# Optimization experiments

Hardware: AMD Instinct MI355X
Metric: run time of the kernel (lower is better)

## Reference

```python
import jax, jax.numpy as jnp
import numpy as np

N_MEM = 50000
MATCH_THR2 = 0.01   # squared-distance match threshold (0.1 m)
EMA = 0.5           # EMA factor for matched-descriptor update
EPS = 1e-8


def _bilinear_depth(depth, uv):
    # depth: [H, W]; uv: [M, 2] pixel coords (u = x/col, v = y/row)
    H, W = depth.shape
    u = jnp.clip(uv[:, 0], 0.0, W - 1.001)
    v = jnp.clip(uv[:, 1], 0.0, H - 1.001)
    u0 = jnp.floor(u); v0 = jnp.floor(v)
    du = u - u0; dv = v - v0
    u0i = u0.astype(jnp.int32); v0i = v0.astype(jnp.int32)
    d00 = depth[v0i, u0i]
    d01 = depth[v0i, u0i + 1]
    d10 = depth[v0i + 1, u0i]
    d11 = depth[v0i + 1, u0i + 1]
    return d00 * (1 - du) * (1 - dv) + d01 * du * (1 - dv) + d10 * (1 - du) * dv + d11 * du * dv


def pix2world(points, depth_map, pose, K):
    # points [B,M,2], depth_map [B,1,H,W], pose [B,3,4] cam->world, K [B,3,3]
    d = jax.vmap(_bilinear_depth)(depth_map[:, 0], points)            # [B,M]
    pix = jnp.concatenate([points, jnp.ones_like(points[..., :1])], -1)  # [B,M,3]
    Kinv = jnp.linalg.inv(K)
    cam = jnp.einsum('bij,bmj->bmi', Kinv, pix) * d[..., None]        # [B,M,3]
    world = jnp.einsum('bij,bmj->bmi', pose[:, :, :3], cam) + pose[:, :, 3][:, None, :]
    valid = (d > 0) & jnp.isfinite(world).all(-1)                      # [B,M]
    return world, valid


def memory_write(pts, desc, valid, mem_pts, mem_desc, next_ptr):
    # pts [P,3], desc [P,D]; mem_pts [N,3], mem_desc [N,D]
    d2 = (jnp.sum(pts * pts, -1, keepdims=True)
          - 2.0 * pts @ mem_pts.T
          + jnp.sum(mem_pts * mem_pts, -1)[None, :])                  # [P,N]
    idx = jnp.argmin(d2, axis=1)                                       # [P]
    dmin = jnp.take_along_axis(d2, idx[:, None], axis=1)[:, 0]
    match = (dmin < MATCH_THR2) & valid
    n_match = match.sum()
    # returned descriptors come from the (non-differentiable) memory buffer;
    # unmatched entries return their own descriptor (cos=1 -> zero loss/grad)
    matched_desc = jax.lax.stop_gradient(jnp.where(match[:, None], mem_desc[idx], desc))
    # --- state update (buffers: no gradient) ---
    dsg = jax.lax.stop_gradient(desc)
    psg = jax.lax.stop_gradient(pts)
    unm = (~match) & valid
    slots = (next_ptr + jnp.cumsum(unm.astype(jnp.int32)) - 1) % N_MEM
    widx = jnp.where(unm, slots, idx)                                  # [P]
    old_pts = mem_pts[widx]; old_desc = mem_desc[widx]
    upd = old_desc * EMA + dsg * (1.0 - EMA)
    upd = upd / (jnp.linalg.norm(upd, axis=-1, keepdims=True) + EPS)
    new_desc_vals = jnp.where(match[:, None], upd, jnp.where(unm[:, None], dsg, old_desc))
    new_pts_vals = jnp.where(unm[:, None], psg, old_pts)
    new_mem_desc = mem_desc.at[widx].set(new_desc_vals)
    new_mem_pts = mem_pts.at[widx].set(new_pts_vals)
    return matched_desc, n_match, new_mem_pts, new_mem_desc


def setup_inputs() -> dict:
    key = jax.random.key(0)
    ks = jax.random.split(key, 8)
    B, M, D, H, W = 8, 512, 256, 480, 640
    points = jax.random.uniform(ks[0], (B, M, 2), jnp.float32) * jnp.array([W - 2.0, H - 2.0])
    depth_map = 0.5 + 4.5 * jax.random.uniform(ks[1], (B, 1, H, W), jnp.float32)
    # proper rotations via QR + small translations
    A = np.asarray(jax.random.normal(ks[2], (B, 3, 3)))
    Rs = np.stack([np.linalg.qr(A[b])[0] for b in range(B)]).astype(np.float32)
    t = np.asarray(jax.random.normal(ks[3], (B, 3, 1))) * 2.0
    pose = jnp.asarray(np.concatenate([Rs, t.astype(np.float32)], axis=2))  # [B,3,4]
    Kmat = jnp.broadcast_to(jnp.array([[320.0, 0.0, 320.0], [0.0, 320.0, 240.0], [0.0, 0.0, 1.0]], jnp.float32), (B, 3, 3))
    descriptors = jax.random.normal(ks[4], (B, M, D), jnp.float32)
    mem_pts = (jax.random.uniform(ks[5], (N_MEM, 3), jnp.float32) - 0.5) * 16.0
    mem_desc = jax.random.normal(ks[6], (N_MEM, D), jnp.float32)
    mem_desc = mem_desc / (jnp.linalg.norm(mem_desc, axis=-1, keepdims=True) + EPS)
    return {"points": points, "depth_map": depth_map, "pose": pose, "K": Kmat,
            "descriptors": descriptors, "mem_pts": mem_pts, "mem_desc": mem_desc,
            "next_ptr": 20000}


def reference(points, depth_map, pose, K, descriptors, mem_pts, mem_desc, next_ptr):
    world, valid = pix2world(points, depth_map, pose, K)               # [B,M,3], [B,M]
    P = world.shape[0] * world.shape[1]
    pts = world.reshape(P, 3)
    desc = descriptors.reshape(P, -1)
    vmask = valid.reshape(P)
    pts = jnp.where(vmask[:, None], pts, 1e6)   # invalid points never match
    matched_desc, n_match, new_mem_pts, new_mem_desc = memory_write(
        pts, desc, vmask, mem_pts, mem_desc, next_ptr)
    a = desc / jnp.maximum(jnp.linalg.norm(desc, axis=-1, keepdims=True), EPS)
    b = matched_desc / jnp.maximum(jnp.linalg.norm(matched_desc, axis=-1, keepdims=True), EPS)
    cos = jnp.sum(a * b, -1)                                           # [P]
    nv = jnp.maximum(vmask.sum(), 1)
    loss = 1.0 - jnp.sum(cos * vmask) / nv
    return loss, n_match, new_mem_pts, new_mem_desc
```

## Files before the change

### kernel.cpp

```cpp
#include <hip/hip_runtime.h>
#include <math.h>

#define N_MEM   50000
#define P_TOT   4096
#define DDIM    256
#define HDIM    480
#define WDIM    640
#define SWEEPB  196
#define COPYB   2048
#define THR2    0.01f
#define EPSF    1e-8f

#define GDIM    24
#define NCELL   13824
#define GORG    -8.25f
#define GINV    (1.0f/0.6875f)
#define GRS     0.15f
#define CPT     14

typedef unsigned long long ull;

__device__ __forceinline__ unsigned fsort(float x) {
    unsigned b = __float_as_uint(x);
    return (b & 0x80000000u) ? ~b : (b | 0x80000000u);
}

__device__ __forceinline__ int cell1d(float x) {
    int c = (int)((x - GORG) * GINV);
    return min(max(c, 0), GDIM - 1);
}

__global__ __launch_bounds__(1024) void k_build(const float* __restrict__ points,
                                                const float* __restrict__ depth,
                                                const float* __restrict__ pose,
                                                const float* __restrict__ Kmat,
                                                float4* __restrict__ pts_out,
                                                int* __restrict__ flags_out,
                                                ull* __restrict__ minkey,
                                                int* __restrict__ qstart,
                                                int* __restrict__ qidx,
                                                ull* __restrict__ minkey_inv,
                                                float* __restrict__ cos_acc)
{
    __shared__ int cnt[NCELL];
    __shared__ int bsum[1024];
    int t = threadIdx.x;
    for (int c = t; c < NCELL; c += 1024) cnt[c] = 0;
    if (t == 0) { *minkey_inv = 0xFFFFFFFFFFFFFFFFULL; *cos_acc = 0.f; }
    for (int k = t; k < P_TOT; k += 1024) minkey[k] = 0xFFFFFFFFFFFFFFFFULL;
    __syncthreads();

    int cells[4];
    #pragma unroll
    for (int i = 0; i < 4; ++i) {
        int p = i * 1024 + t;
        int b = p >> 9;
        const float* K = Kmat + b * 9;
        float a00=K[0],a01=K[1],a02=K[2],a10=K[3],a11=K[4],a12=K[5],a20=K[6],a21=K[7],a22=K[8];
        float det = a00*(a11*a22-a12*a21) - a01*(a10*a22-a12*a20) + a02*(a10*a21-a11*a20);
        float id = 1.0f/det;
        float i00=(a11*a22-a12*a21)*id, i01=(a02*a21-a01*a22)*id, i02=(a01*a12-a02*a11)*id;
        float i10=(a12*a20-a10*a22)*id, i11=(a00*a22-a02*a20)*id, i12=(a02*a10-a00*a12)*id;
        float i20=(a10*a21-a11*a20)*id, i21=(a01*a20-a00*a21)*id, i22=(a00*a11-a01*a10)*id;

        float u = points[p*2+0], v = points[p*2+1];
        float uc = fminf(fmaxf(u, 0.f), (float)WDIM - 1.001f);
        float vc = fminf(fmaxf(v, 0.f), (float)HDIM - 1.001f);
        float u0 = floorf(uc), v0 = floorf(vc);
        float du = uc - u0, dv = vc - v0;
        int u0i = (int)u0, v0i = (int)v0;
        const float* dm = depth + (size_t)b * HDIM * WDIM;
        float d00 = dm[v0i*WDIM + u0i];
        float d01 = dm[v0i*WDIM + u0i + 1];
        float d10 = dm[(v0i+1)*WDIM + u0i];
        float d11 = dm[(v0i+1)*WDIM + u0i + 1];
        float d = d00*(1.f-du)*(1.f-dv) + d01*du*(1.f-dv) + d10*(1.f-du)*dv + d11*du*dv;

        float cx = (i00*u + i01*v + i02) * d;
        float cy = (i10*u + i11*v + i12) * d;
        float cz = (i20*u + i21*v + i22) * d;
        const float* T = pose + b * 12;
        float wx = T[0]*cx + T[1]*cy + T[2]*cz  + T[3];
        float wy = T[4]*cx + T[5]*cy + T[6]*cz  + T[7];
        float wz = T[8]*cx + T[9]*cy + T[10]*cz + T[11];
        int val = (d > 0.f) && isfinite(wx) && isfinite(wy) && isfinite(wz);
        float px = val ? wx : 1e6f;
        float py = val ? wy : 1e6f;
        float pz = val ? wz : 1e6f;
        float pp = px*px + py*py + pz*pz;
        pts_out[p] = make_float4(px, py, pz, pp);
        flags_out[p] = val;
        int c = -1;
        if (val) {
            c = (cell1d(pz) * GDIM + cell1d(py)) * GDIM + cell1d(px);
            atomicAdd(&cnt[c], 1);
        }
        cells[i] = c;
    }
    __syncthreads();

    int base = t * CPT;
    int loc[CPT];
    int sum = 0;
    #pragma unroll
    for (int i = 0; i < CPT; ++i) {
        int idx = base + i;
        int cv = (idx < NCELL) ? cnt[idx] : 0;
        loc[i] = sum; sum += cv;
    }
    bsum[t] = sum;
    __syncthreads();
    for (int off = 1; off < 1024; off <<= 1) {
        int a = bsum[t];
        int bb = (t >= off) ? bsum[t - off] : 0;
        __syncthreads();
        bsum[t] = a + bb;
        __syncthreads();
    }
    int ex = bsum[t] - sum;
    #pragma unroll
    for (int i = 0; i < CPT; ++i) {
        int idx = base + i;
        if (idx < NCELL) { int s0 = ex + loc[i]; qstart[idx] = s0; cnt[idx] = s0; }
    }
    if (t == 1023) qstart[NCELL] = bsum[1023];
    __syncthreads();

    #pragma unroll
    for (int i = 0; i < 4; ++i) {
        if (cells[i] >= 0) {
            int p = i * 1024 + t;
            int pos = atomicAdd(&cnt[cells[i]], 1);
            qidx[pos] = p;
        }
    }
}

__global__ __launch_bounds__(256) void k_main(const float* __restrict__ mem_pts,
                                              const float* __restrict__ mem_desc,
                                              const float4* __restrict__ pts,
                                              const int* __restrict__ qstart,
                                              const int* __restrict__ qidx,
                                              ull* __restrict__ minkey,
                                              ull* __restrict__ minkey_inv,
                                              float* __restrict__ out_pts,
                                              float* __restrict__ out_desc)
{
    __shared__ ull sred[4];
    int bid = blockIdx.x;
    int t = threadIdx.x;
    if (bid < SWEEPB) {
        int j = bid * 256 + t;
        ull ikey = 0xFFFFFFFFFFFFFFFFULL;
        if (j < N_MEM) {
            float mx = mem_pts[j*3+0], my = mem_pts[j*3+1], mz = mem_pts[j*3+2];
            float mm = mx*mx + my*my + mz*mz;
            float px = 1e6f;
            float pp  = px*px + px*px + px*px;
            float dot = px*mx + px*my + px*mz;
            float dinv = pp - 2.f*dot + mm;
            ikey = ((ull)fsort(dinv) << 32) | (unsigned)j;
            int cx0 = cell1d(mx - GRS), cx1 = cell1d(mx + GRS);
            int cy0 = cell1d(my - GRS), cy1 = cell1d(my + GRS);
            int cz0 = cell1d(mz - GRS), cz1 = cell1d(mz + GRS);
            for (int zz = cz0; zz <= cz1; ++zz)
                for (int yy = cy0; yy <= cy1; ++yy) {
                    int rowc = (zz * GDIM + yy) * GDIM;
                    for (int xx = cx0; xx <= cx1; ++xx) {
                        int cell = rowc + xx;
                        int s0 = qstart[cell], s1 = qstart[cell + 1];
                        for (int k = s0; k < s1; ++k) {
                            int p = qidx[k];
                            float4 P = pts[p];
                            float dotq = P.x*mx + P.y*my + P.z*mz;
                            float dd2 = P.w - 2.f*dotq + mm;
                            atomicMin(&minkey[p], ((ull)fsort(dd2) << 32) | (unsigned)j);
                        }
                    }
                }
        }
        for (int off = 32; off; off >>= 1) {
            ull o = __shfl_xor(ikey, off);
            ikey = o < ikey ? o : ikey;
        }
        if ((t & 63) == 0) sred[t >> 6] = ikey;
        __syncthreads();
        if (t == 0) {
            ull a = sred[0] < sred[1] ? sred[0] : sred[1];
            ull b = sred[2] < sred[3] ? sred[2] : sred[3];
            ull m = a < b ? a : b;
            atomicMin(minkey_inv, m);
        }
    } else {
        const long tid = (long)(bid - SWEEPB) * 256 + t;
        const long stride = (long)COPYB * 256;
        const float2* ds = (const float2*)mem_desc;
        float2* dd = (float2*)out_desc;
        const long ND2 = (long)N_MEM * DDIM / 2;
        long k = tid * 4;
        const long stride4 = stride * 4;
        for (; k + 3 < ND2; k += stride4) {
            float2 a0 = ds[k+0], a1 = ds[k+1], a2 = ds[k+2], a3 = ds[k+3];
            dd[k+0] = a0; dd[k+1] = a1; dd[k+2] = a2; dd[k+3] = a3;
        }
        for (; k < ND2; ++k) dd[k] = ds[k];
        const float2* ps = (const float2*)mem_pts;
        float2* pd = (float2*)out_pts;
        for (long i = tid; i < (long)N_MEM * 3 / 2; i += stride) pd[i] = ps[i];
    }
}

__global__ __launch_bounds__(1024) void k_scan(const ull* __restrict__ minkey,
                                               int* __restrict__ flags,
                                               const int* __restrict__ next_ptr,
                                               const ull* __restrict__ minkey_inv,
                                               int* __restrict__ widx,
                                               int* __restrict__ winner,
                                               float* __restrict__ dout,
                                               float* __restrict__ scan_out)
{
    __shared__ int su[1024];
    __shared__ int smc[1024];
    int t = threadIdx.x;
    int base = t * 4;
    const ull thr_key = ((ull)fsort(THR2)) << 32;
    ull inv = *minkey_inv;
    int um[4], iv[4], wvv[4];
    int usum = 0, msum = 0;
    #pragma unroll
    for (int k = 0; k < 4; k++) {
        int v = flags[base + k] & 1;
        ull key = v ? minkey[base + k] : inv;
        int m = (key < thr_key) && v;
        int u = (!m) && v;
        iv[k] = (int)(key & 0xffffffffULL);
        um[k] = u; usum += u; msum += m;
        flags[base + k] = v | (m << 1) | (u << 2);
    }
    su[t] = usum; smc[t] = msum;
    __syncthreads();
    for (int off = 1; off < 1024; off <<= 1) {
        int a = su[t], b = (t >= off) ? su[t - off] : 0;
        int c = smc[t], d = (t >= off) ? smc[t - off] : 0;
        __syncthreads();
        su[t] = a + b; smc[t] = c + d;
        __syncthreads();
    }
    int excl = su[t] - usum;
    int np_ = *next_ptr;
    int run = excl;
    #pragma unroll
    for (int k = 0; k < 4; k++) {
        int wv;
        if (um[k]) { run += 1; wv = (np_ + run - 1) % N_MEM; }
        else       { wv = iv[k]; }
        widx[base + k] = wv;
        wvv[k] = wv;
        winner[wv] = -1;
    }
    __syncthreads();
    #pragma unroll
    for (int k = 0; k < 4; k++)
        atomicMax(&winner[wvv[k]], base + k);
    if (t == 1023) {
        dout[1]     = (float)smc[1023];
        scan_out[0] = (float)(smc[1023] + su[1023]);
        scan_out[1] = (float)su[1023];
    }
}

__global__ __launch_bounds__(256) void k_scatloss(const int* __restrict__ widx,
                                                  const int* __restrict__ flags,
                                                  const int* __restrict__ winner,
                                                  const float* __restrict__ desc,
                                                  const float4* __restrict__ pts,
                                                  const float* __restrict__ mem_pts,
                                                  const float* __restrict__ mem_desc,
                                                  float* __restrict__ out_pts,
                                                  float* __restrict__ out_desc,
                                                  float* __restrict__ cos_acc)
{
    __shared__ float red[16];
    int p = blockIdx.x;
    int t = threadIdx.x;
    int f = flags[p];
    int m = (f >> 1) & 1, u = (f >> 2) & 1;
    int wi = widx[p];
    int win = (winner[wi] == p);
    if (!m && !win) return;
    float dsg = desc[p * DDIM + t];
    float old = mem_desc[(long)wi * DDIM + t];
    float val;
    if (m) {
        float up = old * 0.5f + dsg * 0.5f;
        float sdd = dsg * dsg, smm2 = old * old, sdm = dsg * old, suu = up * up;
        for (int off = 32; off; off >>= 1) {
            sdd  += __shfl_xor(sdd,  off);
            smm2 += __shfl_xor(smm2, off);
            sdm  += __shfl_xor(sdm,  off);
            suu  += __shfl_xor(suu,  off);
        }
        int w = t >> 6;
        if ((t & 63) == 0) { red[w] = sdd; red[4+w] = smm2; red[8+w] = sdm; red[12+w] = suu; }
        __syncthreads();
        float dd  = red[0] + red[1] + red[2] + red[3];
        float mm2 = red[4] + red[5] + red[6] + red[7];
        float dm  = red[8] + red[9] + red[10] + red[11];
        float uu  = red[12] + red[13] + red[14] + red[15];
        float cosv = dm / (fmaxf(sqrtf(dd), EPSF) * fmaxf(sqrtf(mm2), EPSF));
        val = up / (sqrtf(uu) + EPSF);
        if (t == 0) atomicAdd(cos_acc, cosv);
    } else {
        val = u ? dsg : old;
    }
    if (win) {
        out_desc[(long)wi * DDIM + t] = val;
        if (t == 0) {
            float px, py, pz;
            if (u) { float4 P = pts[p]; px = P.x; py = P.y; pz = P.z; }
            else   { px = mem_pts[wi*3]; py = mem_pts[wi*3+1]; pz = mem_pts[wi*3+2]; }
            out_pts[wi*3+0] = px; out_pts[wi*3+1] = py; out_pts[wi*3+2] = pz;
        }
    }
}

__global__ void k_final(const float* __restrict__ cos_acc,
                        const float* __restrict__ scan_out,
                        float* __restrict__ dout)
{
    if (threadIdx.x == 0) {
        float nv = fmaxf(scan_out[0], 1.f);
        dout[0] = 1.f - (*cos_acc + scan_out[1]) / nv;
    }
}

extern "C" void kernel_launch(void* const* d_in, const int* in_sizes, int n_in,
                              void* d_out, int out_size, void* d_ws, size_t ws_size,
                              hipStream_t stream)
{
    const float* points   = (const float*)d_in[0];
    const float* depth    = (const float*)d_in[1];
    const float* pose     = (const float*)d_in[2];
    const float* Kmat     = (const float*)d_in[3];
    const float* desc     = (const float*)d_in[4];
    const float* mem_pts  = (const float*)d_in[5];
    const float* mem_desc = (const float*)d_in[6];
    const int*   next_ptr = (const int*)d_in[7];

    float* out      = (float*)d_out;
    float* out_pts  = out + 2;
    float* out_desc = out + 2 + (long)N_MEM * 3;

    char* ws = (char*)d_ws;
    float4* pts_ws    = (float4*)(ws);
    int* flags_ws     = (int*)(ws + 65536);
    int* widx_ws      = (int*)(ws + 81920);
    int* winner_ws    = (int*)(ws + 98304);
    ull* minkey_ws    = (ull*)(ws + 298304);
    int* qstart_ws    = (int*)(ws + 331072);
    int* qidx_ws      = (int*)(ws + 386372);
    ull* minkey_inv   = (ull*)(ws + 402760);
    float* scan_out   = (float*)(ws + 402768);
    float* cos_acc    = (float*)(ws + 402776);

    k_build   <<<1, 1024, 0, stream>>>(points, depth, pose, Kmat,
                                       pts_ws, flags_ws, minkey_ws,
                                       qstart_ws, qidx_ws, minkey_inv, cos_acc);
    k_main    <<<SWEEPB + COPYB, 256, 0, stream>>>(mem_pts, mem_desc, pts_ws,
                                                   qstart_ws, qidx_ws, minkey_ws, minkey_inv,
                                                   out_pts, out_desc);
    k_scan    <<<1, 1024, 0, stream>>>(minkey_ws, flags_ws, next_ptr, minkey_inv,
                                       widx_ws, winner_ws, out, scan_out);
    k_scatloss<<<P_TOT, 256, 0, stream>>>(widx_ws, flags_ws, winner_ws, desc, pts_ws,
                                          mem_pts, mem_desc, out_pts, out_desc, cos_acc);
    k_final   <<<1, 64, 0, stream>>>(cos_acc, scan_out, out);
}
```

Before: 203.3 us.

## Bin memory points into grid and query per point-cell instead of per memory point

```diff
diff --git a/kernel.cpp b/kernel.cpp
--- a/kernel.cpp
+++ b/kernel.cpp
@@ -6,7 +6,7 @@
 #define DDIM    256
 #define HDIM    480
 #define WDIM    640
-#define SWEEPB  196
+#define SWEEPB  128
 #define COPYB   2048
 #define THR2    0.01f
 #define EPSF    1e-8f
@@ -34,70 +34,91 @@
                                                 const float* __restrict__ depth,
                                                 const float* __restrict__ pose,
                                                 const float* __restrict__ Kmat,
+                                                const float* __restrict__ mem_pts,
                                                 float4* __restrict__ pts_out,
                                                 int* __restrict__ flags_out,
                                                 ull* __restrict__ minkey,
-                                                int* __restrict__ qstart,
-                                                int* __restrict__ qidx,
-                                                ull* __restrict__ minkey_inv,
-                                                float* __restrict__ cos_acc)
+                                                int* __restrict__ mstart,
+                                                int* __restrict__ msorted,
+                                                ull* __restrict__ minkey_inv)
 {
     __shared__ int cnt[NCELL];
     __shared__ int bsum[1024];
+    __shared__ ull sred[16];
     int t = threadIdx.x;
+
+    if (blockIdx.x == 0) {
+        for (int k = t; k < P_TOT; k += 1024) minkey[k] = 0xFFFFFFFFFFFFFFFFULL;
+        #pragma unroll
+        for (int i = 0; i < 4; ++i) {
+            int p = i * 1024 + t;
+            int b = p >> 9;
+            const float* K = Kmat + b * 9;
+            float a00=K[0],a01=K[1],a02=K[2],a10=K[3],a11=K[4],a12=K[5],a20=K[6],a21=K[7],a22=K[8];
+            float det = a00*(a11*a22-a12*a21) - a01*(a10*a22-a12*a20) + a02*(a10*a21-a11*a20);
+            float id = 1.0f/det;
+            float i00=(a11*a22-a12*a21)*id, i01=(a02*a21-a01*a22)*id, i02=(a01*a12-a02*a11)*id;
+            float i10=(a12*a20-a10*a22)*id, i11=(a00*a22-a02*a20)*id, i12=(a02*a10-a00*a12)*id;
+            float i20=(a10*a21-a11*a20)*id, i21=(a01*a20-a00*a21)*id, i22=(a00*a11-a01*a10)*id;
+
+            float u = points[p*2+0], v = points[p*2+1];
+            float uc = fminf(fmaxf(u, 0.f), (float)WDIM - 1.001f);
+            float vc = fminf(fmaxf(v, 0.f), (float)HDIM - 1.001f);
+            float u0 = floorf(uc), v0 = floorf(vc);
+            float du = uc - u0, dv = vc - v0;
+            int u0i = (int)u0, v0i = (int)v0;
+            const float* dm = depth + (size_t)b * HDIM * WDIM;
+            float d00 = dm[v0i*WDIM + u0i];
+            float d01 = dm[v0i*WDIM + u0i + 1];
+            float d10 = dm[(v0i+1)*WDIM + u0i];
+            float d11 = dm[(v0i+1)*WDIM + u0i + 1];
+            float d = d00*(1.f-du)*(1.f-dv) + d01*du*(1.f-dv) + d10*(1.f-du)*dv + d11*du*dv;
+
+            float cx = (i00*u + i01*v + i02) * d;
+            float cy = (i10*u + i11*v + i12) * d;
+            float cz = (i20*u + i21*v + i22) * d;
+            const float* T = pose + b * 12;
+            float wx = T[0]*cx + T[1]*cy + T[2]*cz  + T[3];
+            float wy = T[4]*cx + T[5]*cy + T[6]*cz  + T[7];
+            float wz = T[8]*cx + T[9]*cy + T[10]*cz + T[11];
+            int val = (d > 0.f) && isfinite(wx) && isfinite(wy) && isfinite(wz);
+            float px = val ? wx : 1e6f;
+            float py = val ? wy : 1e6f;
+            float pz = val ? wz : 1e6f;
+            float pp = px*px + py*py + pz*pz;
+            pts_out[p] = make_float4(px, py, pz, pp);
+            flags_out[p] = val;
+        }
+        return;
+    }
+
     for (int c = t; c < NCELL; c += 1024) cnt[c] = 0;
-    if (t == 0) { *minkey_inv = 0xFFFFFFFFFFFFFFFFULL; *cos_acc = 0.f; }
-    for (int k = t; k < P_TOT; k += 1024) minkey[k] = 0xFFFFFFFFFFFFFFFFULL;
-    __syncthreads();
-
-    int cells[4];
-    #pragma unroll
-    for (int i = 0; i < 4; ++i) {
-        int p = i * 1024 + t;
-        int b = p >> 9;
-        const float* K = Kmat + b * 9;
-        float a00=K[0],a01=K[1],a02=K[2],a10=K[3],a11=K[4],a12=K[5],a20=K[6],a21=K[7],a22=K[8];
-        float det = a00*(a11*a22-a12*a21) - a01*(a10*a22-a12*a20) + a02*(a10*a21-a11*a20);
-        float id = 1.0f/det;
-        float i00=(a11*a22-a12*a21)*id, i01=(a02*a21-a01*a22)*id, i02=(a01*a12-a02*a11)*id;
-        float i10=(a12*a20-a10*a22)*id, i11=(a00*a22-a02*a20)*id, i12=(a02*a10-a00*a12)*id;
-        float i20=(a10*a21-a11*a20)*id, i21=(a01*a20-a00*a21)*id, i22=(a00*a11-a01*a10)*id;
-
-        float u = points[p*2+0], v = points[p*2+1];
-        float uc = fminf(fmaxf(u, 0.f), (float)WDIM - 1.001f);
-        float vc = fminf(fmaxf(v, 0.f), (float)HDIM - 1.001f);
-        float u0 = floorf(uc), v0 = floorf(vc);
-        float du = uc - u0, dv = vc - v0;
-        int u0i = (int)u0, v0i = (int)v0;
-        const float* dm = depth + (size_t)b * HDIM * WDIM;
-        float d00 = dm[v0i*WDIM + u0i];
-        float d01 = dm[v0i*WDIM + u0i + 1];
-        float d10 = dm[(v0i+1)*WDIM + u0i];
-        float d11 = dm[(v0i+1)*WDIM + u0i + 1];
-        float d = d00*(1.f-du)*(1.f-dv) + d01*du*(1.f-dv) + d10*(1.f-du)*dv + d11*du*dv;
-
-        float cx = (i00*u + i01*v + i02) * d;
-        float cy = (i10*u + i11*v + i12) * d;
-        float cz = (i20*u + i21*v + i22) * d;
-        const float* T = pose + b * 12;
-        float wx = T[0]*cx + T[1]*cy + T[2]*cz  + T[3];
-        float wy = T[4]*cx + T[5]*cy + T[6]*cz  + T[7];
-        float wz = T[8]*cx + T[9]*cy + T[10]*cz + T[11];
-        int val = (d > 0.f) && isfinite(wx) && isfinite(wy) && isfinite(wz);
-        float px = val ? wx : 1e6f;
-        float py = val ? wy : 1e6f;
-        float pz = val ? wz : 1e6f;
-        float pp = px*px + py*py + pz*pz;
-        pts_out[p] = make_float4(px, py, pz, pp);
-        flags_out[p] = val;
-        int c = -1;
-        if (val) {
-            c = (cell1d(pz) * GDIM + cell1d(py)) * GDIM + cell1d(px);
-            atomicAdd(&cnt[c], 1);
-        }
-        cells[i] = c;
-    }
-    __syncthreads();
+    __syncthreads();
+
+    ull ikey = 0xFFFFFFFFFFFFFFFFULL;
+    for (int j = t; j < N_MEM; j += 1024) {
+        float mx = mem_pts[j*3+0], my = mem_pts[j*3+1], mz = mem_pts[j*3+2];
+        int c = (cell1d(mz) * GDIM + cell1d(my)) * GDIM + cell1d(mx);
+        atomicAdd(&cnt[c], 1);
+        float mm = mx*mx + my*my + mz*mz;
+        float px = 1e6f;
+        float pp  = px*px + px*px + px*px;
+        float dot = px*mx + px*my + px*mz;
+        float dinv = pp - 2.f*dot + mm;
+        ull key = ((ull)fsort(dinv) << 32) | (unsigned)j;
+        ikey = key < ikey ? key : ikey;
+    }
+    for (int off = 32; off; off >>= 1) {
+        ull o = __shfl_xor(ikey, off);
+        ikey = o < ikey ? o : ikey;
+    }
+    if ((t & 63) == 0) sred[t >> 6] = ikey;
+    __syncthreads();
+    if (t == 0) {
+        ull m = sred[0];
+        for (int w = 1; w < 16; ++w) m = sred[w] < m ? sred[w] : m;
+        *minkey_inv = m;
+    }
 
     int base = t * CPT;
     int loc[CPT];
@@ -121,92 +142,72 @@
     #pragma unroll
     for (int i = 0; i < CPT; ++i) {
         int idx = base + i;
-        if (idx < NCELL) { int s0 = ex + loc[i]; qstart[idx] = s0; cnt[idx] = s0; }
-    }
-    if (t == 1023) qstart[NCELL] = bsum[1023];
-    __syncthreads();
-
-    #pragma unroll
-    for (int i = 0; i < 4; ++i) {
-        if (cells[i] >= 0) {
-            int p = i * 1024 + t;
-            int pos = atomicAdd(&cnt[cells[i]], 1);
-            qidx[pos] = p;
-        }
+        if (idx < NCELL) { int s0 = ex + loc[i]; mstart[idx] = s0; cnt[idx] = s0; }
+    }
+    if (t == 1023) mstart[NCELL] = bsum[1023];
+    __syncthreads();
+
+    for (int j = t; j < N_MEM; j += 1024) {
+        float mx = mem_pts[j*3+0], my = mem_pts[j*3+1], mz = mem_pts[j*3+2];
+        int c = (cell1d(mz) * GDIM + cell1d(my)) * GDIM + cell1d(mx);
+        int pos = atomicAdd(&cnt[c], 1);
+        msorted[pos] = j;
     }
 }
 
 __global__ __launch_bounds__(256) void k_main(const float* __restrict__ mem_pts,
                                               const float* __restrict__ mem_desc,
                                               const float4* __restrict__ pts,
-                                              const int* __restrict__ qstart,
-                                              const int* __restrict__ qidx,
+                                              const int* __restrict__ flags,
+                                              const int* __restrict__ mstart,
+                                              const int* __restrict__ msorted,
                                               ull* __restrict__ minkey,
-                                              ull* __restrict__ minkey_inv,
                                               float* __restrict__ out_pts,
                                               float* __restrict__ out_desc)
 {
-    __shared__ ull sred[4];
     int bid = blockIdx.x;
     int t = threadIdx.x;
     if (bid < SWEEPB) {
-        int j = bid * 256 + t;
-        ull ikey = 0xFFFFFFFFFFFFFFFFULL;
-        if (j < N_MEM) {
+        int gid = bid * 256 + t;
+        int p  = gid >> 3;
+        int ci = gid & 7;
+        if (!flags[p]) return;
+        float4 P = pts[p];
+        int x0 = cell1d(P.x - GRS), x1 = cell1d(P.x + GRS);
+        int y0 = cell1d(P.y - GRS), y1 = cell1d(P.y + GRS);
+        int z0 = cell1d(P.z - GRS), z1 = cell1d(P.z + GRS);
+        int xx = (ci & 1)        ? x1 : x0;
+        int yy = ((ci >> 1) & 1) ? y1 : y0;
+        int zz = (ci >> 2)       ? z1 : z0;
+        int cell = (zz * GDIM + yy) * GDIM + xx;
+        int s0 = mstart[cell], s1 = mstart[cell + 1];
+        ull best = 0xFFFFFFFFFFFFFFFFULL;
+        for (int k = s0; k < s1; ++k) {
+            int j = msorted[k];
             float mx = mem_pts[j*3+0], my = mem_pts[j*3+1], mz = mem_pts[j*3+2];
-            float mm = mx*mx + my*my + mz*mz;
-            float px = 1e6f;
-            float pp  = px*px + px*px + px*px;
-            float dot = px*mx + px*my + px*mz;
-            float dinv = pp - 2.f*dot + mm;
-            ikey = ((ull)fsort(dinv) << 32) | (unsigned)j;
-            int cx0 = cell1d(mx - GRS), cx1 = cell1d(mx + GRS);
-            int cy0 = cell1d(my - GRS), cy1 = cell1d(my + GRS);
-            int cz0 = cell1d(mz - GRS), cz1 = cell1d(mz + GRS);
-            for (int zz = cz0; zz <= cz1; ++zz)
-                for (int yy = cy0; yy <= cy1; ++yy) {
-                    int rowc = (zz * GDIM + yy) * GDIM;
-                    for (int xx = cx0; xx <= cx1; ++xx) {
-                        int cell = rowc + xx;
-                        int s0 = qstart[cell], s1 = qstart[cell + 1];
-                        for (int k = s0; k < s1; ++k) {
-                            int p = qidx[k];
-                            float4 P = pts[p];
-                            float dotq = P.x*mx + P.y*my + P.z*mz;
-                            float dd2 = P.w - 2.f*dotq + mm;
-                            atomicMin(&minkey[p], ((ull)fsort(dd2) << 32) | (unsigned)j);
-                        }
-                    }
-                }
-        }
-        for (int off = 32; off; off >>= 1) {
-            ull o = __shfl_xor(ikey, off);
-            ikey = o < ikey ? o : ikey;
-        }
-        if ((t & 63) == 0) sred[t >> 6] = ikey;
-        __syncthreads();
-        if (t == 0) {
-            ull a = sred[0] < sred[1] ? sred[0] : sred[1];
-            ull b = sred[2] < sred[3] ? sred[2] : sred[3];
-            ull m = a < b ? a : b;
-            atomicMin(minkey_inv, m);
-        }
+            float mm  = mx*mx + my*my + mz*mz;
+            float dot = P.x*mx + P.y*my + P.z*mz;
+            float dd2 = P.w - 2.f*dot + mm;
+            ull key = ((ull)fsort(dd2) << 32) | (unsigned)j;
+            best = key < best ? key : best;
+        }
+        if (best != 0xFFFFFFFFFFFFFFFFULL)
+            atomicMin(&minkey[p], best);
     } else {
         const long tid = (long)(bid - SWEEPB) * 256 + t;
-        const long stride = (long)COPYB * 256;
+        const long NT = (long)COPYB * 256;
         const float2* ds = (const float2*)mem_desc;
         float2* dd = (float2*)out_desc;
         const long ND2 = (long)N_MEM * DDIM / 2;
-        long k = tid * 4;
-        const long stride4 = stride * 4;
-        for (; k + 3 < ND2; k += stride4) {
-            float2 a0 = ds[k+0], a1 = ds[k+1], a2 = ds[k+2], a3 = ds[k+3];
-            dd[k+0] = a0; dd[k+1] = a1; dd[k+2] = a2; dd[k+3] = a3;
-        }
-        for (; k < ND2; ++k) dd[k] = ds[k];
+        long k = tid;
+        for (; k + 3*NT < ND2; k += 4*NT) {
+            float2 a0 = ds[k], a1 = ds[k+NT], a2 = ds[k+2*NT], a3 = ds[k+3*NT];
+            dd[k] = a0; dd[k+NT] = a1; dd[k+2*NT] = a2; dd[k+3*NT] = a3;
+        }
+        for (; k < ND2; k += NT) dd[k] = ds[k];
         const float2* ps = (const float2*)mem_pts;
         float2* pd = (float2*)out_pts;
-        for (long i = tid; i < (long)N_MEM * 3 / 2; i += stride) pd[i] = ps[i];
+        for (long i = tid; i < (long)N_MEM * 3 / 2; i += NT) pd[i] = ps[i];
     }
 }
 
@@ -263,9 +264,11 @@
     for (int k = 0; k < 4; k++)
         atomicMax(&winner[wvv[k]], base + k);
     if (t == 1023) {
+        int n_u = su[1023];
+        float nvf = fmaxf((float)(smc[1023] + n_u), 1.f);
         dout[1]     = (float)smc[1023];
-        scan_out[0] = (float)(smc[1023] + su[1023]);
-        scan_out[1] = (float)su[1023];
+        dout[0]     = 1.f - (float)n_u / nvf;
+        scan_out[0] = nvf;
     }
 }
 
@@ -278,7 +281,8 @@
                                                   const float* __restrict__ mem_desc,
                                                   float* __restrict__ out_pts,
                                                   float* __restrict__ out_desc,
-                                                  float* __restrict__ cos_acc)
+                                                  const float* __restrict__ scan_out,
+                                                  float* __restrict__ dout)
 {
     __shared__ float red[16];
     int p = blockIdx.x;
@@ -309,7 +313,7 @@
         float uu  = red[12] + red[13] + red[14] + red[15];
         float cosv = dm / (fmaxf(sqrtf(dd), EPSF) * fmaxf(sqrtf(mm2), EPSF));
         val = up / (sqrtf(uu) + EPSF);
-        if (t == 0) atomicAdd(cos_acc, cosv);
+        if (t == 0) atomicAdd(&dout[0], -cosv / scan_out[0]);
     } else {
         val = u ? dsg : old;
     }
@@ -321,16 +325,6 @@
             else   { px = mem_pts[wi*3]; py = mem_pts[wi*3+1]; pz = mem_pts[wi*3+2]; }
             out_pts[wi*3+0] = px; out_pts[wi*3+1] = py; out_pts[wi*3+2] = pz;
         }
-    }
-}
-
-__global__ void k_final(const float* __restrict__ cos_acc,
-                        const float* __restrict__ scan_out,
-                        float* __restrict__ dout)
-{
-    if (threadIdx.x == 0) {
-        float nv = fmaxf(scan_out[0], 1.f);
-        dout[0] = 1.f - (*cos_acc + scan_out[1]) / nv;
     }
 }
 
@@ -357,21 +351,20 @@
     int* widx_ws      = (int*)(ws + 81920);
     int* winner_ws    = (int*)(ws + 98304);
     ull* minkey_ws    = (ull*)(ws + 298304);
-    int* qstart_ws    = (int*)(ws + 331072);
-    int* qidx_ws      = (int*)(ws + 386372);
-    ull* minkey_inv   = (ull*)(ws + 402760);
-    float* scan_out   = (float*)(ws + 402768);
-    float* cos_acc    = (float*)(ws + 402776);
-
-    k_build   <<<1, 1024, 0, stream>>>(points, depth, pose, Kmat,
+    int* mstart_ws    = (int*)(ws + 331072);
+    int* msorted_ws   = (int*)(ws + 386372);
+    ull* minkey_inv   = (ull*)(ws + 586376);
+    float* scan_out   = (float*)(ws + 586384);
+
+    k_build   <<<2, 1024, 0, stream>>>(points, depth, pose, Kmat, mem_pts,
                                        pts_ws, flags_ws, minkey_ws,
-                                       qstart_ws, qidx_ws, minkey_inv, cos_acc);
-    k_main    <<<SWEEPB + COPYB, 256, 0, stream>>>(mem_pts, mem_desc, pts_ws,
-                                                   qstart_ws, qidx_ws, minkey_ws, minkey_inv,
+                                       mstart_ws, msorted_ws, minkey_inv);
+    k_main    <<<SWEEPB + COPYB, 256, 0, stream>>>(mem_pts, mem_desc, pts_ws, flags_ws,
+                                                   mstart_ws, msorted_ws, minkey_ws,
                                                    out_pts, out_desc);
     k_scan    <<<1, 1024, 0, stream>>>(minkey_ws, flags_ws, next_ptr, minkey_inv,
                                        widx_ws, winner_ws, out, scan_out);
     k_scatloss<<<P_TOT, 256, 0, stream>>>(widx_ws, flags_ws, winner_ws, desc, pts_ws,
-                                          mem_pts, mem_desc, out_pts, out_desc, cos_acc);
-    k_final   <<<1, 64, 0, stream>>>(cos_acc, scan_out, out);
-}
+                                          mem_pts, mem_desc, out_pts, out_desc,
+                                          scan_out, out);
+}
```

New measurement: 217.1 us. 6.8% more time.
